# Optimization experiments

Hardware: AMD Instinct MI355X
Metric: run time of the kernel (lower is better)

Reference implementation:

```python
import jax, jax.numpy as jnp
import numpy as np

N = 50000      # num_nodes
E = 800000     # num_edges (before self loops)
EMB = 128      # emb_dim
GH = 64        # gcn_hidden
TD = 4         # temporal_dim
B = 64         # batch of sequences
T = 200        # max sequence length
H = 128        # lstm_hidden (per direction)
IN_DIM = 2 + EMB + TD


def lstm_scan(x_tbi, w_ih, w_hh, b_ih, b_hh):
    """x_tbi: [T, B, I] -> hidden states [T, B, H]. PyTorch gate order i,f,g,o."""
    Bsz = x_tbi.shape[1]
    Hh = w_hh.shape[1]

    def step(carry, xt):
        h, c = carry
        g = xt @ w_ih.T + h @ w_hh.T + b_ih + b_hh
        i, f, gg, o = jnp.split(g, 4, axis=-1)
        c = jax.nn.sigmoid(f) * c + jax.nn.sigmoid(i) * jnp.tanh(gg)
        h = jax.nn.sigmoid(o) * jnp.tanh(c)
        return (h, c), h

    init = (jnp.zeros((Bsz, Hh), x_tbi.dtype), jnp.zeros((Bsz, Hh), x_tbi.dtype))
    _, hs = jax.lax.scan(step, init, x_tbi)
    return hs


def gcn_layer(x, W, b, src, dst, ew):
    """PyG GCNConv: linear -> symmetric-norm gather/scatter-add -> bias.
    (self loops already appended to src/dst/ew by caller)"""
    h = x @ W  # [N, out]
    deg = jax.ops.segment_sum(ew, dst, num_segments=N)
    dinv = jnp.where(deg > 0, jax.lax.rsqrt(deg), 0.0)
    norm = dinv[src] * ew * dinv[dst]            # [E+N]
    msg = h[src] * norm[:, None]                  # gather + scale
    return jax.ops.segment_sum(msg, dst, num_segments=N) + b


def setup_inputs() -> dict:
    key = jax.random.key(0)
    ks = jax.random.split(key, 16)
    s = 0.02
    return {
        'x_coords': jax.random.normal(ks[0], (N, 2), jnp.float32),
        'temporal_features': jax.random.uniform(ks[1], (N, TD), jnp.float32, -1.0, 1.0),
        'edge_index': jax.random.randint(ks[2], (2, E), 0, N),
        'edge_weight': jnp.ones((E,), jnp.float32),
        'seq': jax.random.randint(ks[3], (B, T), 0, N),
        'lengths': jax.random.randint(ks[4], (B,), 1, T + 1),
        'node_emb': jax.random.normal(ks[5], (N, EMB), jnp.float32) * s,
        'gcn1_w': jax.random.normal(ks[6], (IN_DIM, GH), jnp.float32) * s,
        'gcn1_b': jnp.zeros((GH,), jnp.float32),
        'gcn2_w': jax.random.normal(ks[7], (GH, EMB), jnp.float32) * s,
        'gcn2_b': jnp.zeros((EMB,), jnp.float32),
        'w_ih_f': jax.random.normal(ks[8], (4 * H, EMB), jnp.float32) * s,
        'w_hh_f': jax.random.normal(ks[9], (4 * H, H), jnp.float32) * s,
        'b_ih_f': jnp.zeros((4 * H,), jnp.float32),
        'b_hh_f': jnp.zeros((4 * H,), jnp.float32),
        'w_ih_b': jax.random.normal(ks[10], (4 * H, EMB), jnp.float32) * s,
        'w_hh_b': jax.random.normal(ks[11], (4 * H, H), jnp.float32) * s,
        'b_ih_b': jnp.zeros((4 * H,), jnp.float32),
        'b_hh_b': jnp.zeros((4 * H,), jnp.float32),
        'attn_w': jax.random.normal(ks[12], (2 * H,), jnp.float32) * s,
        'attn_b': jnp.zeros((), jnp.float32),
        'fc_w': jax.random.normal(ks[13], (2 * H, N), jnp.float32) * s,
        'fc_b': jnp.zeros((N,), jnp.float32),
    }


def reference(x_coords, temporal_features, edge_index, edge_weight, seq, lengths,
              node_emb, gcn1_w, gcn1_b, gcn2_w, gcn2_b,
              w_ih_f, w_hh_f, b_ih_f, b_hh_f,
              w_ih_b, w_hh_b, b_ih_b, b_hh_b,
              attn_w, attn_b, fc_w, fc_b):
    # --- GCN with self loops (PyG add_self_loops=True, fill_value=1) ---
    loop = jnp.arange(N)
    src = jnp.concatenate([edge_index[0], loop])
    dst = jnp.concatenate([edge_index[1], loop])
    ew = jnp.concatenate([edge_weight, jnp.ones((N,), edge_weight.dtype)])

    x = jnp.concatenate([x_coords, node_emb, temporal_features], axis=1)  # [N, 134]
    z = jax.nn.relu(gcn_layer(x, gcn1_w, gcn1_b, src, dst, ew))
    z = gcn_layer(z, gcn2_w, gcn2_b, src, dst, ew)  # dropout = identity (eval)

    # --- sequence embedding + BiLSTM ---
    seq_emb = z[seq]                                  # [B, T, EMB]
    h_f = lstm_scan(seq_emb.transpose(1, 0, 2), w_ih_f, w_hh_f, b_ih_f, b_hh_f)
    h_f = h_f.transpose(1, 0, 2)                      # [B, T, H]

    # backward direction: reverse each sequence within its valid length
    t = jnp.arange(T)
    valid = t[None, :] < lengths[:, None]             # [B, T]
    rev_idx = jnp.where(valid, lengths[:, None] - 1 - t[None, :], t[None, :])
    x_rev = jnp.take_along_axis(seq_emb, rev_idx[:, :, None], axis=1)
    h_b = lstm_scan(x_rev.transpose(1, 0, 2), w_ih_b, w_hh_b, b_ih_b, b_hh_b)
    h_b = jnp.take_along_axis(h_b.transpose(1, 0, 2), rev_idx[:, :, None], axis=1)

    lstm_out = jnp.concatenate([h_f, h_b], axis=-1)   # [B, T, 2H]

    # --- masked attention pooling ---
    scores = lstm_out @ attn_w + attn_b               # [B, T]
    scores = jnp.where(valid, scores, -jnp.inf)
    aw = jax.nn.softmax(scores, axis=1)
    context = jnp.einsum('bt,btd->bd', aw, lstm_out)  # [B, 2H]

    return context @ fc_w + fc_b                      # [B, N]
```

## Files before the change

kernel.cpp:

```cpp
#include <hip/hip_runtime.h>
#include <math.h>

#define NN 50000
#define NE 800000
#define EMB 128
#define GH 64
#define BB 64
#define TT 200
#define HH 128
#define G4 512
#define IND 134

__device__ __forceinline__ float sigf(float x) { return 1.0f / (1.0f + __expf(-x)); }
__device__ __forceinline__ float tanhf_(float x) { return 1.0f - 2.0f / (__expf(2.0f * x) + 1.0f); }
__device__ __forceinline__ void fma4(float4& a, float s, const float4 w) {
    a.x += s * w.x; a.y += s * w.y; a.z += s * w.z; a.w += s * w.w;
}

__global__ void hist_kernel(const int* __restrict__ ei, const float* __restrict__ ew,
                            int* __restrict__ cnt, float* __restrict__ degw) {
    int e = blockIdx.x * 256 + threadIdx.x;
    if (e >= NE) return;
    int d = ei[NE + e];
    atomicAdd(&cnt[d], 1);
    atomicAdd(&degw[d], ew[e]);
}

__global__ void dinv_kernel(const float* __restrict__ degw, float* __restrict__ dinv) {
    int n = blockIdx.x * 256 + threadIdx.x;
    if (n >= NN) return;
    dinv[n] = rsqrtf(degw[n] + 1.0f);
}

__global__ __launch_bounds__(1024) void scan1_kernel(const int* __restrict__ cnt,
                                                     int* __restrict__ rs, int* __restrict__ partials) {
    __shared__ int s[1024];
    int gid = blockIdx.x * 1024 + threadIdx.x;
    int v = (gid < NN) ? cnt[gid] : 0;
    s[threadIdx.x] = v;
    __syncthreads();
    for (int off = 1; off < 1024; off <<= 1) {
        int add = (threadIdx.x >= (unsigned)off) ? s[threadIdx.x - off] : 0;
        __syncthreads();
        s[threadIdx.x] += add;
        __syncthreads();
    }
    if (gid < NN) rs[gid] = s[threadIdx.x] - v;
    if (threadIdx.x == 1023) partials[blockIdx.x] = s[1023];
}

__global__ void scan2_kernel(int* __restrict__ partials, int nblk) {
    if (threadIdx.x == 0) {
        int acc = 0;
        for (int i = 0; i < nblk; ++i) { int v = partials[i]; partials[i] = acc; acc += v; }
    }
}

__global__ __launch_bounds__(1024) void scan3_kernel(const int* __restrict__ partials,
                                                     int* __restrict__ rs, int* __restrict__ cursor) {
    int gid = blockIdx.x * 1024 + threadIdx.x;
    if (gid < NN) {
        int v = rs[gid] + partials[gid >> 10];
        rs[gid] = v;
        cursor[gid] = v;
    }
    if (gid == 0) rs[NN] = NE;
}

__global__ void fill_kernel(const int* __restrict__ ei, const float* __restrict__ ew,
                            const float* __restrict__ dinv, int* __restrict__ cursor,
                            int* __restrict__ ssrc, float* __restrict__ sw) {
    int e = blockIdx.x * 256 + threadIdx.x;
    if (e >= NE) return;
    int s = ei[e], d = ei[NE + e];
    int pos = atomicAdd(&cursor[d], 1);
    ssrc[pos] = s;
    sw[pos] = ew[e] * dinv[s] * dinv[d];
}

__global__ __launch_bounds__(256) void gemm1_kernel(const float* __restrict__ coords,
                                                    const float* __restrict__ temporal,
                                                    const float* __restrict__ emb,
                                                    const float* __restrict__ W1,
                                                    float* __restrict__ h1) {
    __shared__ __align__(16) float wl[IND][GH];
    for (int i = threadIdx.x; i < IND * GH / 4; i += 256)
        ((float4*)wl)[i] = ((const float4*)W1)[i];
    __syncthreads();
    int n = blockIdx.x * 256 + threadIdx.x;
    if (n >= NN) return;
    float4 acc[16];
    float c0 = coords[2 * n], c1 = coords[2 * n + 1];
#pragma unroll
    for (int j = 0; j < 16; ++j) {
        float4 wa = *(const float4*)&wl[0][j * 4];
        float4 wb = *(const float4*)&wl[1][j * 4];
        float4 a;
        a.x = c0 * wa.x + c1 * wb.x; a.y = c0 * wa.y + c1 * wb.y;
        a.z = c0 * wa.z + c1 * wb.z; a.w = c0 * wa.w + c1 * wb.w;
        acc[j] = a;
    }
    const float4* er = (const float4*)(emb + (size_t)n * EMB);
#pragma unroll 2
    for (int k4 = 0; k4 < 32; ++k4) {
        float4 v = er[k4];
        int k = 2 + k4 * 4;
#pragma unroll
        for (int j = 0; j < 16; ++j) {
            fma4(acc[j], v.x, *(const float4*)&wl[k][j * 4]);
            fma4(acc[j], v.y, *(const float4*)&wl[k + 1][j * 4]);
            fma4(acc[j], v.z, *(const float4*)&wl[k + 2][j * 4]);
            fma4(acc[j], v.w, *(const float4*)&wl[k + 3][j * 4]);
        }
    }
    float t0 = temporal[4 * n], t1 = temporal[4 * n + 1], t2 = temporal[4 * n + 2], t3 = temporal[4 * n + 3];
#pragma unroll
    for (int j = 0; j < 16; ++j) {
        fma4(acc[j], t0, *(const float4*)&wl[130][j * 4]);
        fma4(acc[j], t1, *(const float4*)&wl[131][j * 4]);
        fma4(acc[j], t2, *(const float4*)&wl[132][j * 4]);
        fma4(acc[j], t3, *(const float4*)&wl[133][j * 4]);
        *(float4*)&h1[(size_t)n * GH + j * 4] = acc[j];
    }
}

__global__ __launch_bounds__(256) void agg_kernel(const float* __restrict__ hin,
                                                  const int* __restrict__ rs,
                                                  const int* __restrict__ ssrc,
                                                  const float* __restrict__ sw,
                                                  const float* __restrict__ dinv,
                                                  const float* __restrict__ bias, int relu,
                                                  float* __restrict__ hout) {
    int lane = threadIdx.x & 63;
    int wid = threadIdx.x >> 6;
    int n = blockIdx.x * 4 + wid;
    if (n >= NN) return;
    float dv = dinv[n];
    float acc = hin[(size_t)n * GH + lane] * (dv * dv);
    int i = rs[n], e1 = rs[n + 1];
    for (; i + 3 < e1; i += 4) {
        int s0 = ssrc[i], s1 = ssrc[i + 1], s2 = ssrc[i + 2], s3 = ssrc[i + 3];
        float w0 = sw[i], w1 = sw[i + 1], w2 = sw[i + 2], w3 = sw[i + 3];
        float a0 = hin[(size_t)s0 * GH + lane];
        float a1 = hin[(size_t)s1 * GH + lane];
        float a2 = hin[(size_t)s2 * GH + lane];
        float a3 = hin[(size_t)s3 * GH + lane];
        acc += a0 * w0 + a1 * w1 + a2 * w2 + a3 * w3;
    }
    for (; i < e1; ++i) acc += hin[(size_t)ssrc[i] * GH + lane] * sw[i];
    if (bias) acc += bias[lane];
    if (relu) acc = fmaxf(acc, 0.0f);
    hout[(size_t)n * GH + lane] = acc;
}

__global__ __launch_bounds__(256) void gemm2_kernel(const float* __restrict__ a2,
                                                    const float* __restrict__ W2,
                                                    const float* __restrict__ b2,
                                                    float* __restrict__ z2) {
    __shared__ __align__(16) float wl[GH][64];
    int j0 = blockIdx.y * 64;
    for (int i = threadIdx.x; i < GH * 16; i += 256) {
        int k = i >> 4, j4 = i & 15;
        *(float4*)&wl[k][j4 * 4] = *(const float4*)&W2[(size_t)k * EMB + j0 + j4 * 4];
    }
    __syncthreads();
    int n = blockIdx.x * 256 + threadIdx.x;
    if (n >= NN) return;
    float4 acc[16];
#pragma unroll
    for (int j = 0; j < 16; ++j) acc[j] = *(const float4*)&b2[j0 + j * 4];
    const float4* ar = (const float4*)(a2 + (size_t)n * GH);
#pragma unroll 2
    for (int k4 = 0; k4 < 16; ++k4) {
        float4 v = ar[k4];
        int k = k4 * 4;
#pragma unroll
        for (int j = 0; j < 16; ++j) {
            fma4(acc[j], v.x, *(const float4*)&wl[k][j * 4]);
            fma4(acc[j], v.y, *(const float4*)&wl[k + 1][j * 4]);
            fma4(acc[j], v.z, *(const float4*)&wl[k + 2][j * 4]);
            fma4(acc[j], v.w, *(const float4*)&wl[k + 3][j * 4]);
        }
    }
#pragma unroll
    for (int j = 0; j < 16; ++j)
        *(float4*)&z2[(size_t)n * EMB + j0 + j * 4] = acc[j];
}

__global__ void gather_kernel(const int* __restrict__ seq, const float* __restrict__ z2,
                              float* __restrict__ se) {
    int idx = blockIdx.x * 256 + threadIdx.x;
    if (idx >= BB * TT * 32) return;
    int r = idx >> 5, q = idx & 31;
    int node = seq[r];
    ((float4*)se)[(size_t)r * 32 + q] = ((const float4*)z2)[(size_t)node * 32 + q];
}

__global__ __launch_bounds__(256) void pregemm_kernel(const float* __restrict__ se,
                                                      const float* __restrict__ w_ih_f,
                                                      const float* __restrict__ w_ih_b,
                                                      const float* __restrict__ b_ih_f,
                                                      const float* __restrict__ b_hh_f,
                                                      const float* __restrict__ b_ih_b,
                                                      const float* __restrict__ b_hh_b,
                                                      const int* __restrict__ lengths,
                                                      float* __restrict__ xpf,
                                                      float* __restrict__ xpb) {
    int dir = blockIdx.z;
    const float* w_ih = dir ? w_ih_b : w_ih_f;
    int u0 = blockIdx.y * 64;
    __shared__ __align__(16) float wl[64][EMB];
    __shared__ float bs[64];
    {
        const float4* src = (const float4*)(w_ih + (size_t)u0 * EMB);
        for (int i = threadIdx.x; i < 64 * EMB / 4; i += 256) ((float4*)wl)[i] = src[i];
        if (threadIdx.x < 64) {
            int u = u0 + threadIdx.x;
            bs[threadIdx.x] = dir ? (b_ih_b[u] + b_hh_b[u]) : (b_ih_f[u] + b_hh_f[u]);
        }
    }
    __syncthreads();
    int m = blockIdx.x * 256 + threadIdx.x;
    if (m >= TT * BB) return;
    int t = m >> 6, b = m & 63;
    int tsrc = t;
    if (dir) {
        int len = lengths[b];
        if (t >= len) return;
        tsrc = len - 1 - t;
    }
    const float4* row = (const float4*)(se + ((size_t)b * TT + tsrc) * EMB);
    float accs[64];
#pragma unroll
    for (int j = 0; j < 64; ++j) accs[j] = bs[j];
#pragma unroll 2
    for (int k4 = 0; k4 < 32; ++k4) {
        float4 xv = row[k4];
#pragma unroll
        for (int j = 0; j < 64; ++j) {
            float4 wv = *(const float4*)&wl[j][k4 * 4];
            accs[j] += xv.x * wv.x + xv.y * wv.y + xv.z * wv.z + xv.w * wv.w;
        }
    }
    float* xp = dir ? xpb : xpf;
#pragma unroll
    for (int j4 = 0; j4 < 16; ++j4) {
        float4 o = make_float4(accs[j4 * 4], accs[j4 * 4 + 1], accs[j4 * 4 + 2], accs[j4 * 4 + 3]);
        *(float4*)&xp[(size_t)m * G4 + u0 + j4 * 4] = o;
    }
}

__global__ __launch_bounds__(512) void lstm_kernel(const float* __restrict__ xpf,
                                                   const float* __restrict__ xpb,
                                                   const float* __restrict__ w_hh_f,
                                                   const float* __restrict__ w_hh_b,
                                                   const int* __restrict__ lengths,
                                                   float* __restrict__ hfo,
                                                   float* __restrict__ hbo) {
    int chain = blockIdx.x;
    int dir = chain & 1, b = chain >> 1;
    const float* w_hh = dir ? w_hh_b : w_hh_f;
    const float* xp = dir ? xpb : xpf;
    float* ho = dir ? hbo : hfo;
    int u = threadIdx.x;
    int len = lengths[b];
    float w[HH];
    {
        const float4* wr = (const float4*)(w_hh + (size_t)u * HH);
#pragma unroll
        for (int k4 = 0; k4 < 32; ++k4) {
            float4 v = wr[k4];
            w[k4 * 4] = v.x; w[k4 * 4 + 1] = v.y; w[k4 * 4 + 2] = v.z; w[k4 * 4 + 3] = v.w;
        }
    }
    __shared__ __align__(16) float hl[HH];
    __shared__ float gl[G4];
    float c = 0.0f;
    if (u < HH) hl[u] = 0.0f;
    __syncthreads();
    for (int t = 0; t < len; ++t) {
        float acc = xp[((size_t)t * BB + b) * G4 + u];
#pragma unroll
        for (int k4 = 0; k4 < 32; ++k4) {
            float4 hv = *(const float4*)&hl[k4 * 4];
            acc += w[k4 * 4] * hv.x + w[k4 * 4 + 1] * hv.y + w[k4 * 4 + 2] * hv.z + w[k4 * 4 + 3] * hv.w;
        }
        gl[u] = acc;
        __syncthreads();
        if (u < HH) {
            float gi = sigf(gl[u]);
            float gf = sigf(gl[HH + u]);
            float gg = tanhf_(gl[2 * HH + u]);
            float go = sigf(gl[3 * HH + u]);
            c = gf * c + gi * gg;
            float h = go * tanhf_(c);
            int tt = dir ? (len - 1 - t) : t;
            ho[((size_t)b * TT + tt) * HH + u] = h;
            hl[u] = h;
        }
        __syncthreads();
    }
}

__global__ __launch_bounds__(256) void attn_kernel(const float* __restrict__ hf,
                                                   const float* __restrict__ hb,
                                                   const float* __restrict__ attn_w,
                                                   const float* __restrict__ attn_b,
                                                   const int* __restrict__ lengths,
                                                   float* __restrict__ ctx) {
    int b = blockIdx.x;
    int tid = threadIdx.x;
    int len = lengths[b];
    __shared__ __align__(16) float wl[256];
    __shared__ float pl[256];
    __shared__ float red[256];
    wl[tid] = attn_w[tid];
    __syncthreads();
    float sc = -3.0e38f;
    if (tid < len) {
        const float4* rf = (const float4*)(hf + ((size_t)b * TT + tid) * HH);
        const float4* rb = (const float4*)(hb + ((size_t)b * TT + tid) * HH);
        const float4* w4 = (const float4*)wl;
        float s = attn_b[0];
        for (int k4 = 0; k4 < 32; ++k4) {
            float4 a = rf[k4], ww = w4[k4];
            s += a.x * ww.x + a.y * ww.y + a.z * ww.z + a.w * ww.w;
        }
        for (int k4 = 0; k4 < 32; ++k4) {
            float4 a = rb[k4], ww = w4[32 + k4];
            s += a.x * ww.x + a.y * ww.y + a.z * ww.z + a.w * ww.w;
        }
        sc = s;
    }
    red[tid] = sc;
    __syncthreads();
    for (int off = 128; off > 0; off >>= 1) {
        if (tid < off) red[tid] = fmaxf(red[tid], red[tid + off]);
        __syncthreads();
    }
    float mx = red[0];
    __syncthreads();
    float e = (tid < len) ? __expf(sc - mx) : 0.0f;
    red[tid] = e;
    __syncthreads();
    for (int off = 128; off > 0; off >>= 1) {
        if (tid < off) red[tid] += red[tid + off];
        __syncthreads();
    }
    float inv = 1.0f / red[0];
    pl[tid] = e * inv;
    __syncthreads();
    float acc = 0.0f;
    const float* basep = (tid < HH) ? (hf + (size_t)b * TT * HH + tid)
                                    : (hb + (size_t)b * TT * HH + (tid - HH));
    for (int t = 0; t < len; ++t) acc += pl[t] * basep[(size_t)t * HH];
    ctx[(size_t)b * 256 + tid] = acc;
}

__global__ __launch_bounds__(256) void fc_kernel(const float* __restrict__ ctx,
                                                 const float* __restrict__ fc_w,
                                                 const float* __restrict__ fc_b,
                                                 float* __restrict__ out) {
    __shared__ __align__(16) float cl[64][256];
    for (int i = threadIdx.x; i < 64 * 256 / 4; i += 256)
        ((float4*)cl)[i] = ((const float4*)ctx)[i];
    __syncthreads();
    int nb = threadIdx.x & 63;
    int bq = threadIdx.x >> 6;
    int n = blockIdx.x * 64 + nb;
    if (n >= NN) return;
    float acc[16];
#pragma unroll
    for (int i = 0; i < 16; ++i) acc[i] = 0.0f;
#pragma unroll 2
    for (int k4 = 0; k4 < 64; ++k4) {
        int k = k4 * 4;
        float w0 = fc_w[(size_t)k * NN + n];
        float w1 = fc_w[(size_t)(k + 1) * NN + n];
        float w2 = fc_w[(size_t)(k + 2) * NN + n];
        float w3 = fc_w[(size_t)(k + 3) * NN + n];
#pragma unroll
        for (int i = 0; i < 16; ++i) {
            float4 cv = *(const float4*)&cl[bq * 16 + i][k];
            acc[i] += cv.x * w0 + cv.y * w1 + cv.z * w2 + cv.w * w3;
        }
    }
    float fb = fc_b[n];
#pragma unroll
    for (int i = 0; i < 16; ++i)
        out[(size_t)(bq * 16 + i) * NN + n] = acc[i] + fb;
}

extern "C" void kernel_launch(void* const* d_in, const int* in_sizes, int n_in,
                              void* d_out, int out_size, void* d_ws, size_t ws_size,
                              hipStream_t stream) {
    const float* x_coords   = (const float*)d_in[0];
    const float* temporal   = (const float*)d_in[1];
    const int*   edge_index = (const int*)d_in[2];
    const float* edge_w     = (const float*)d_in[3];
    const int*   seq        = (const int*)d_in[4];
    const int*   lengths    = (const int*)d_in[5];
    const float* node_emb   = (const float*)d_in[6];
    const float* gcn1_w     = (const float*)d_in[7];
    const float* gcn1_b     = (const float*)d_in[8];
    const float* gcn2_w     = (const float*)d_in[9];
    const float* gcn2_b     = (const float*)d_in[10];
    const float* w_ih_f     = (const float*)d_in[11];
    const float* w_hh_f     = (const float*)d_in[12];
    const float* b_ih_f     = (const float*)d_in[13];
    const float* b_hh_f     = (const float*)d_in[14];
    const float* w_ih_b     = (const float*)d_in[15];
    const float* w_hh_b     = (const float*)d_in[16];
    const float* b_ih_b     = (const float*)d_in[17];
    const float* b_hh_b     = (const float*)d_in[18];
    const float* attn_w     = (const float*)d_in[19];
    const float* attn_b     = (const float*)d_in[20];
    const float* fc_w       = (const float*)d_in[21];
    const float* fc_b       = (const float*)d_in[22];
    float* out = (float*)d_out;

    char* base = (char*)d_ws;
    size_t off = 0;
    auto alloc = [&](size_t nbytes) -> void* {
        void* p = base + off;
        off = (off + nbytes + 255) & ~(size_t)255;
        return p;
    };
    int*   cnt     = (int*)alloc((size_t)2 * NN * 4);
    float* degw    = (float*)(cnt + NN);
    float* dinv    = (float*)alloc((size_t)NN * 4);
    int*   rs      = (int*)alloc(((size_t)NN + 1) * 4);
    int*   cursor  = (int*)alloc((size_t)NN * 4);
    int*   partials= (int*)alloc(64 * 4);
    int*   ssrc    = (int*)alloc((size_t)NE * 4);
    float* sw      = (float*)alloc((size_t)NE * 4);
    float* h1      = (float*)alloc((size_t)NN * GH * 4);
    float* z1      = (float*)alloc((size_t)NN * GH * 4);
    float* a2      = h1;
    float* z2      = (float*)alloc((size_t)NN * EMB * 4);
    float* se      = (float*)alloc((size_t)BB * TT * EMB * 4);
    float* xpf     = (float*)alloc((size_t)TT * BB * G4 * 4);
    float* xpb     = (float*)alloc((size_t)TT * BB * G4 * 4);
    float* hfo     = (float*)alloc((size_t)BB * TT * HH * 4);
    float* hbo     = (float*)alloc((size_t)BB * TT * HH * 4);
    float* ctx     = (float*)alloc((size_t)BB * 256 * 4);
    (void)ws_size; (void)in_sizes; (void)n_in; (void)out_size;

    hipMemsetAsync(cnt, 0, (size_t)2 * NN * 4, stream);

    hist_kernel<<<(NE + 255) / 256, 256, 0, stream>>>(edge_index, edge_w, cnt, degw);
    dinv_kernel<<<(NN + 255) / 256, 256, 0, stream>>>(degw, dinv);
    const int nblk = (NN + 1023) / 1024;
    scan1_kernel<<<nblk, 1024, 0, stream>>>(cnt, rs, partials);
    scan2_kernel<<<1, 64, 0, stream>>>(partials, nblk);
    scan3_kernel<<<nblk, 1024, 0, stream>>>(partials, rs, cursor);
    fill_kernel<<<(NE + 255) / 256, 256, 0, stream>>>(edge_index, edge_w, dinv, cursor, ssrc, sw);

    gemm1_kernel<<<(NN + 255) / 256, 256, 0, stream>>>(x_coords, temporal, node_emb, gcn1_w, h1);
    agg_kernel<<<(NN + 3) / 4, 256, 0, stream>>>(h1, rs, ssrc, sw, dinv, gcn1_b, 1, z1);
    agg_kernel<<<(NN + 3) / 4, 256, 0, stream>>>(z1, rs, ssrc, sw, dinv, (const float*)nullptr, 0, a2);
    gemm2_kernel<<<dim3((NN + 255) / 256, 2), 256, 0, stream>>>(a2, gcn2_w, gcn2_b, z2);

    gather_kernel<<<(BB * TT * 32 + 255) / 256, 256, 0, stream>>>(seq, z2, se);
    pregemm_kernel<<<dim3(TT * BB / 256, 8, 2), 256, 0, stream>>>(
        se, w_ih_f, w_ih_b, b_ih_f, b_hh_f, b_ih_b, b_hh_b, lengths, xpf, xpb);
    lstm_kernel<<<BB * 2, 512, 0, stream>>>(xpf, xpb, w_hh_f, w_hh_b, lengths, hfo, hbo);
    attn_kernel<<<BB, 256, 0, stream>>>(hfo, hbo, attn_w, attn_b, lengths, ctx);
    fc_kernel<<<(NN + 63) / 64, 256, 0, stream>>>(ctx, fc_w, fc_b, out);
}
```

Baseline: 702.0 us.

## Interleave LSTM gate rows per lane and exchange gates via shuffles

The recurrent LSTM kernel now maps the four gate rows of each hidden unit to four adjacent lanes and combines their pre-activations with warp shuffles. This removes the shared gate buffer and one of the two block barriers per timestep. It also double-buffers the hidden state in shared memory, prefetches the next timestep's input projection, and splits the dot product into four accumulators for more ILP. All four lanes redundantly compute the cell update. A small unroll pragma is added to the attention context loop.

After: 700.4 us. Within noise of the previous version (-0.2%).

```diff
diff --git a/kernel.cpp b/kernel.cpp
--- a/kernel.cpp
+++ b/kernel.cpp
@@ -250,55 +250,64 @@
     }
 }
 
-__global__ __launch_bounds__(512) void lstm_kernel(const float* __restrict__ xpf,
-                                                   const float* __restrict__ xpb,
-                                                   const float* __restrict__ w_hh_f,
-                                                   const float* __restrict__ w_hh_b,
-                                                   const int* __restrict__ lengths,
-                                                   float* __restrict__ hfo,
-                                                   float* __restrict__ hbo) {
+#define LSTM_LW(i) float4 W##i = wr[i];
+#define LSTM_FMA(i) { float4 hv = h4[i]; \
+    a0 += W##i.x * hv.x; a1 += W##i.y * hv.y; a2 += W##i.z * hv.z; a3 += W##i.w * hv.w; }
+
+__global__ __launch_bounds__(512, 1) void lstm_kernel(const float* __restrict__ xpf,
+                                                      const float* __restrict__ xpb,
+                                                      const float* __restrict__ w_hh_f,
+                                                      const float* __restrict__ w_hh_b,
+                                                      const int* __restrict__ lengths,
+                                                      float* __restrict__ hfo,
+                                                      float* __restrict__ hbo) {
     int chain = blockIdx.x;
     int dir = chain & 1, b = chain >> 1;
     const float* w_hh = dir ? w_hh_b : w_hh_f;
     const float* xp = dir ? xpb : xpf;
     float* ho = dir ? hbo : hfo;
-    int u = threadIdx.x;
+    int tid = threadIdx.x;
+    int u = tid >> 2, g = tid & 3;
     int len = lengths[b];
-    float w[HH];
-    {
-        const float4* wr = (const float4*)(w_hh + (size_t)u * HH);
-#pragma unroll
-        for (int k4 = 0; k4 < 32; ++k4) {
-            float4 v = wr[k4];
-            w[k4 * 4] = v.x; w[k4 * 4 + 1] = v.y; w[k4 * 4 + 2] = v.z; w[k4 * 4 + 3] = v.w;
-        }
-    }
-    __shared__ __align__(16) float hl[HH];
-    __shared__ float gl[G4];
-    float c = 0.0f;
-    if (u < HH) hl[u] = 0.0f;
-    __syncthreads();
+
+    const float4* wr = (const float4*)(w_hh + (size_t)(g * HH + u) * HH);
+    LSTM_LW(0) LSTM_LW(1) LSTM_LW(2) LSTM_LW(3) LSTM_LW(4) LSTM_LW(5) LSTM_LW(6) LSTM_LW(7)
+    LSTM_LW(8) LSTM_LW(9) LSTM_LW(10) LSTM_LW(11) LSTM_LW(12) LSTM_LW(13) LSTM_LW(14) LSTM_LW(15)
+    LSTM_LW(16) LSTM_LW(17) LSTM_LW(18) LSTM_LW(19) LSTM_LW(20) LSTM_LW(21) LSTM_LW(22) LSTM_LW(23)
+    LSTM_LW(24) LSTM_LW(25) LSTM_LW(26) LSTM_LW(27) LSTM_LW(28) LSTM_LW(29) LSTM_LW(30) LSTM_LW(31)
+
+    __shared__ __align__(16) float hl[2][HH];
+    if (tid < HH) hl[0][tid] = 0.0f;
+    __syncthreads();
+
+    const float* xpt = xp + (size_t)b * G4 + g * HH + u;
+    float cst = 0.0f;
+    float xcur = xpt[0];
     for (int t = 0; t < len; ++t) {
-        float acc = xp[((size_t)t * BB + b) * G4 + u];
-#pragma unroll
-        for (int k4 = 0; k4 < 32; ++k4) {
-            float4 hv = *(const float4*)&hl[k4 * 4];
-            acc += w[k4 * 4] * hv.x + w[k4 * 4 + 1] * hv.y + w[k4 * 4 + 2] * hv.z + w[k4 * 4 + 3] * hv.w;
-        }
-        gl[u] = acc;
-        __syncthreads();
-        if (u < HH) {
-            float gi = sigf(gl[u]);
-            float gf = sigf(gl[HH + u]);
-            float gg = tanhf_(gl[2 * HH + u]);
-            float go = sigf(gl[3 * HH + u]);
-            c = gf * c + gi * gg;
-            float h = go * tanhf_(c);
+        float xnext = (t + 1 < len) ? xpt[(size_t)(t + 1) * BB * G4] : 0.0f;
+        const float4* h4 = (const float4*)hl[t & 1];
+        float a0 = 0.0f, a1 = 0.0f, a2 = 0.0f, a3 = 0.0f;
+        LSTM_FMA(0) LSTM_FMA(1) LSTM_FMA(2) LSTM_FMA(3) LSTM_FMA(4) LSTM_FMA(5) LSTM_FMA(6) LSTM_FMA(7)
+        LSTM_FMA(8) LSTM_FMA(9) LSTM_FMA(10) LSTM_FMA(11) LSTM_FMA(12) LSTM_FMA(13) LSTM_FMA(14) LSTM_FMA(15)
+        LSTM_FMA(16) LSTM_FMA(17) LSTM_FMA(18) LSTM_FMA(19) LSTM_FMA(20) LSTM_FMA(21) LSTM_FMA(22) LSTM_FMA(23)
+        LSTM_FMA(24) LSTM_FMA(25) LSTM_FMA(26) LSTM_FMA(27) LSTM_FMA(28) LSTM_FMA(29) LSTM_FMA(30) LSTM_FMA(31)
+        float acc = ((a0 + a1) + (a2 + a3)) + xcur;
+        float sb = __shfl_xor(acc, 1, 64);
+        float sc = __shfl_xor(acc, 2, 64);
+        float sd = __shfl_xor(sb, 2, 64);
+        float si = (g == 0) ? acc : (g == 1) ? sb : (g == 2) ? sc : sd;
+        float sf = (g == 0) ? sb : (g == 1) ? acc : (g == 2) ? sd : sc;
+        float sg = (g == 0) ? sc : (g == 1) ? sd : (g == 2) ? acc : sb;
+        float so = (g == 0) ? sd : (g == 1) ? sc : (g == 2) ? sb : acc;
+        cst = sigf(sf) * cst + sigf(si) * tanhf_(sg);
+        float h = sigf(so) * tanhf_(cst);
+        if (g == 0) {
+            hl[(t + 1) & 1][u] = h;
             int tt = dir ? (len - 1 - t) : t;
             ho[((size_t)b * TT + tt) * HH + u] = h;
-            hl[u] = h;
         }
         __syncthreads();
+        xcur = xnext;
     }
 }
 
@@ -353,6 +362,7 @@
     float acc = 0.0f;
     const float* basep = (tid < HH) ? (hf + (size_t)b * TT * HH + tid)
                                     : (hb + (size_t)b * TT * HH + (tid - HH));
+#pragma unroll 4
     for (int t = 0; t < len; ++t) acc += pl[t] * basep[(size_t)t * HH];
     ctx[(size_t)b * 256 + tid] = acc;
 }
```

## Split LSTM recurrence across K-slices and retile input-projection GEMM

Applied to the files above, without the earlier changes.

The LSTM kernel now runs 1024 threads per chain. Each thread holds a 16-wide K-slice of all four gate rows for one hidden unit, and partial sums are reduced through shared memory. The next step's input projection is prefetched while the current step's gates are computed. This cuts per-thread register weight storage (128 floats down to 64) and shortens the serial dot product per step, at the cost of an extra shared-memory reduction per timestep. The pregemm kernel is retiled to 8 output columns by 4 rows per thread, which reduces register pressure and gives more blocks, and the attention time loop is unrolled.

New measurement: 764.1 us. +8.9%, slower.

```diff
diff --git a/kernel.cpp b/kernel.cpp
--- a/kernel.cpp
+++ b/kernel.cpp
@@ -208,95 +208,131 @@
                                                       float* __restrict__ xpb) {
     int dir = blockIdx.z;
     const float* w_ih = dir ? w_ih_b : w_ih_f;
-    int u0 = blockIdx.y * 64;
-    __shared__ __align__(16) float wl[64][EMB];
-    __shared__ float bs[64];
+    int o0 = blockIdx.y * 8;
+    __shared__ __align__(16) float wl[8][EMB];
+    __shared__ float bs[8];
     {
-        const float4* src = (const float4*)(w_ih + (size_t)u0 * EMB);
-        for (int i = threadIdx.x; i < 64 * EMB / 4; i += 256) ((float4*)wl)[i] = src[i];
-        if (threadIdx.x < 64) {
-            int u = u0 + threadIdx.x;
-            bs[threadIdx.x] = dir ? (b_ih_b[u] + b_hh_b[u]) : (b_ih_f[u] + b_hh_f[u]);
-        }
-    }
-    __syncthreads();
-    int m = blockIdx.x * 256 + threadIdx.x;
-    if (m >= TT * BB) return;
-    int t = m >> 6, b = m & 63;
-    int tsrc = t;
-    if (dir) {
-        int len = lengths[b];
-        if (t >= len) return;
-        tsrc = len - 1 - t;
-    }
-    const float4* row = (const float4*)(se + ((size_t)b * TT + tsrc) * EMB);
-    float accs[64];
-#pragma unroll
-    for (int j = 0; j < 64; ++j) accs[j] = bs[j];
-#pragma unroll 2
+        int j = threadIdx.x >> 5, k4 = threadIdx.x & 31;
+        *(float4*)&wl[j][k4 * 4] = *(const float4*)&w_ih[(size_t)(o0 + j) * EMB + k4 * 4];
+        if (threadIdx.x < 8) {
+            int uo = o0 + threadIdx.x;
+            bs[threadIdx.x] = dir ? (b_ih_b[uo] + b_hh_b[uo]) : (b_ih_f[uo] + b_hh_f[uo]);
+        }
+    }
+    __syncthreads();
+    int m0 = blockIdx.x * 1024 + threadIdx.x;
+    const float4* rows[4];
+    bool vstore[4];
+#pragma unroll
+    for (int r = 0; r < 4; ++r) {
+        int m = m0 + 256 * r;
+        bool v = m < TT * BB;
+        int mm = v ? m : 0;
+        int t = mm >> 6, b = mm & 63;
+        int tsrc = t;
+        if (dir) {
+            int len = lengths[b];
+            v = v && (t < len);
+            tsrc = v ? (len - 1 - t) : 0;
+        }
+        vstore[r] = v;
+        rows[r] = (const float4*)(se + ((size_t)b * TT + tsrc) * EMB);
+    }
+    float acc[4][8];
+#pragma unroll
+    for (int r = 0; r < 4; ++r)
+#pragma unroll
+        for (int j = 0; j < 8; ++j) acc[r][j] = bs[j];
     for (int k4 = 0; k4 < 32; ++k4) {
-        float4 xv = row[k4];
-#pragma unroll
-        for (int j = 0; j < 64; ++j) {
+        float4 xv0 = rows[0][k4], xv1 = rows[1][k4], xv2 = rows[2][k4], xv3 = rows[3][k4];
+#pragma unroll
+        for (int j = 0; j < 8; ++j) {
             float4 wv = *(const float4*)&wl[j][k4 * 4];
-            accs[j] += xv.x * wv.x + xv.y * wv.y + xv.z * wv.z + xv.w * wv.w;
+            acc[0][j] += xv0.x * wv.x + xv0.y * wv.y + xv0.z * wv.z + xv0.w * wv.w;
+            acc[1][j] += xv1.x * wv.x + xv1.y * wv.y + xv1.z * wv.z + xv1.w * wv.w;
+            acc[2][j] += xv2.x * wv.x + xv2.y * wv.y + xv2.z * wv.z + xv2.w * wv.w;
+            acc[3][j] += xv3.x * wv.x + xv3.y * wv.y + xv3.z * wv.z + xv3.w * wv.w;
         }
     }
     float* xp = dir ? xpb : xpf;
 #pragma unroll
-    for (int j4 = 0; j4 < 16; ++j4) {
-        float4 o = make_float4(accs[j4 * 4], accs[j4 * 4 + 1], accs[j4 * 4 + 2], accs[j4 * 4 + 3]);
-        *(float4*)&xp[(size_t)m * G4 + u0 + j4 * 4] = o;
-    }
-}
-
-__global__ __launch_bounds__(512) void lstm_kernel(const float* __restrict__ xpf,
-                                                   const float* __restrict__ xpb,
-                                                   const float* __restrict__ w_hh_f,
-                                                   const float* __restrict__ w_hh_b,
-                                                   const int* __restrict__ lengths,
-                                                   float* __restrict__ hfo,
-                                                   float* __restrict__ hbo) {
+    for (int r = 0; r < 4; ++r) {
+        if (!vstore[r]) continue;
+        int m = m0 + 256 * r;
+        float4 oa = make_float4(acc[r][0], acc[r][1], acc[r][2], acc[r][3]);
+        float4 ob = make_float4(acc[r][4], acc[r][5], acc[r][6], acc[r][7]);
+        *(float4*)&xp[(size_t)m * G4 + o0] = oa;
+        *(float4*)&xp[(size_t)m * G4 + o0 + 4] = ob;
+    }
+}
+
+__global__ __launch_bounds__(1024, 4) void lstm_kernel(const float* __restrict__ xpf,
+                                                       const float* __restrict__ xpb,
+                                                       const float* __restrict__ w_hh_f,
+                                                       const float* __restrict__ w_hh_b,
+                                                       const int* __restrict__ lengths,
+                                                       float* __restrict__ hfo,
+                                                       float* __restrict__ hbo) {
     int chain = blockIdx.x;
     int dir = chain & 1, b = chain >> 1;
     const float* w_hh = dir ? w_hh_b : w_hh_f;
     const float* xp = dir ? xpb : xpf;
     float* ho = dir ? hbo : hfo;
-    int u = threadIdx.x;
+    int tid = threadIdx.x;
+    int u = tid & 127;
+    int kq = tid >> 7;
     int len = lengths[b];
-    float w[HH];
-    {
-        const float4* wr = (const float4*)(w_hh + (size_t)u * HH);
-#pragma unroll
-        for (int k4 = 0; k4 < 32; ++k4) {
-            float4 v = wr[k4];
-            w[k4 * 4] = v.x; w[k4 * 4 + 1] = v.y; w[k4 * 4 + 2] = v.z; w[k4 * 4 + 3] = v.w;
-        }
-    }
+
+    float4 W[4][4];
+#pragma unroll
+    for (int g = 0; g < 4; ++g)
+#pragma unroll
+        for (int j4 = 0; j4 < 4; ++j4)
+            W[g][j4] = *(const float4*)&w_hh[(size_t)(g * HH + u) * HH + kq * 16 + j4 * 4];
+
     __shared__ __align__(16) float hl[HH];
-    __shared__ float gl[G4];
-    float c = 0.0f;
-    if (u < HH) hl[u] = 0.0f;
-    __syncthreads();
+    __shared__ __align__(16) float part[HH][9][4];
+    if (tid < HH) hl[tid] = 0.0f;
+    __syncthreads();
+
+    float cst = 0.0f;
+    float x0 = 0.f, x1 = 0.f, x2 = 0.f, x3 = 0.f;
+    const float* xpt = xp + (size_t)b * G4 + u;
+    if (tid < HH && len > 0) {
+        x0 = xpt[0]; x1 = xpt[HH]; x2 = xpt[2 * HH]; x3 = xpt[3 * HH];
+    }
     for (int t = 0; t < len; ++t) {
-        float acc = xp[((size_t)t * BB + b) * G4 + u];
-#pragma unroll
-        for (int k4 = 0; k4 < 32; ++k4) {
-            float4 hv = *(const float4*)&hl[k4 * 4];
-            acc += w[k4 * 4] * hv.x + w[k4 * 4 + 1] * hv.y + w[k4 * 4 + 2] * hv.z + w[k4 * 4 + 3] * hv.w;
-        }
-        gl[u] = acc;
+        const float4* h4 = (const float4*)&hl[kq * 16];
+        float a0 = 0.f, a1 = 0.f, a2 = 0.f, a3 = 0.f;
+#pragma unroll
+        for (int j4 = 0; j4 < 4; ++j4) {
+            float4 hv = h4[j4];
+            a0 += W[0][j4].x * hv.x + W[0][j4].y * hv.y + W[0][j4].z * hv.z + W[0][j4].w * hv.w;
+            a1 += W[1][j4].x * hv.x + W[1][j4].y * hv.y + W[1][j4].z * hv.z + W[1][j4].w * hv.w;
+            a2 += W[2][j4].x * hv.x + W[2][j4].y * hv.y + W[2][j4].z * hv.z + W[2][j4].w * hv.w;
+            a3 += W[3][j4].x * hv.x + W[3][j4].y * hv.y + W[3][j4].z * hv.z + W[3][j4].w * hv.w;
+        }
+        *(float4*)&part[u][kq][0] = make_float4(a0, a1, a2, a3);
         __syncthreads();
-        if (u < HH) {
-            float gi = sigf(gl[u]);
-            float gf = sigf(gl[HH + u]);
-            float gg = tanhf_(gl[2 * HH + u]);
-            float go = sigf(gl[3 * HH + u]);
-            c = gf * c + gi * gg;
-            float h = go * tanhf_(c);
+        if (tid < HH) {
+            float n0 = 0.f, n1 = 0.f, n2 = 0.f, n3 = 0.f;
+            if (t + 1 < len) {
+                const float* xn = xpt + (size_t)(t + 1) * (BB * G4);
+                n0 = xn[0]; n1 = xn[HH]; n2 = xn[2 * HH]; n3 = xn[3 * HH];
+            }
+            float s0 = x0, s1 = x1, s2 = x2, s3 = x3;
+#pragma unroll
+            for (int q = 0; q < 8; ++q) {
+                float4 p = *(const float4*)&part[u][q][0];
+                s0 += p.x; s1 += p.y; s2 += p.z; s3 += p.w;
+            }
+            float gi = sigf(s0), gf = sigf(s1), gg = tanhf_(s2), go = sigf(s3);
+            cst = gf * cst + gi * gg;
+            float h = go * tanhf_(cst);
+            hl[u] = h;
             int tt = dir ? (len - 1 - t) : t;
             ho[((size_t)b * TT + tt) * HH + u] = h;
-            hl[u] = h;
+            x0 = n0; x1 = n1; x2 = n2; x3 = n3;
         }
         __syncthreads();
     }
@@ -353,6 +389,7 @@
     float acc = 0.0f;
     const float* basep = (tid < HH) ? (hf + (size_t)b * TT * HH + tid)
                                     : (hb + (size_t)b * TT * HH + (tid - HH));
+#pragma unroll 4
     for (int t = 0; t < len; ++t) acc += pl[t] * basep[(size_t)t * HH];
     ctx[(size_t)b * 256 + tid] = acc;
 }
@@ -462,9 +499,9 @@
     gemm2_kernel<<<dim3((NN + 255) / 256, 2), 256, 0, stream>>>(a2, gcn2_w, gcn2_b, z2);
 
     gather_kernel<<<(BB * TT * 32 + 255) / 256, 256, 0, stream>>>(seq, z2, se);
-    pregemm_kernel<<<dim3(TT * BB / 256, 8, 2), 256, 0, stream>>>(
+    pregemm_kernel<<<dim3((TT * BB + 1023) / 1024, G4 / 8, 2), 256, 0, stream>>>(
         se, w_ih_f, w_ih_b, b_ih_f, b_hh_f, b_ih_b, b_hh_b, lengths, xpf, xpb);
-    lstm_kernel<<<BB * 2, 512, 0, stream>>>(xpf, xpb, w_hh_f, w_hh_b, lengths, hfo, hbo);
+    lstm_kernel<<<BB * 2, 1024, 0, stream>>>(xpf, xpb, w_hh_f, w_hh_b, lengths, hfo, hbo);
     attn_kernel<<<BB, 256, 0, stream>>>(hfo, hbo, attn_w, attn_b, lengths, ctx);
     fc_kernel<<<(NN + 63) / 64, 256, 0, stream>>>(ctx, fc_w, fc_b, out);
 }
```
